# Kernel optimization log

Measured on AMD Instinct MI355X. Metric: run time of the kernel, lower is better.

Reference implementation:

```python
import jax, jax.numpy as jnp
import numpy as np

G = 128   # long_term_attn_g
H = 8     # num_attn_heads


def setup_inputs() -> dict:
    key = jax.random.key(0)
    ks = jax.random.split(key, 8)
    b, d, t, dk = 8, 1024, 8192, 512  # dk = model_dim // 2
    return {
        "qk": jax.random.normal(ks[0], (b, d, t), jnp.float32),
        "masks": jnp.ones((b, 1, t), jnp.float32),
        "wq": jax.random.normal(ks[1], (dk, d), jnp.float32) * 0.02,
        "bq": jnp.zeros((dk,), jnp.float32),
        "wk": jax.random.normal(ks[2], (dk, d), jnp.float32) * 0.02,
        "bk": jnp.zeros((dk,), jnp.float32),
        "wv": jax.random.normal(ks[3], (dk, d), jnp.float32) * 0.02,
        "bv": jnp.zeros((dk,), jnp.float32),
        "wo": jax.random.normal(ks[4], (d, dk), jnp.float32) * 0.02,
        "bo": jnp.zeros((d,), jnp.float32),
    }


def _to_patches(x, g):
    # convert_to_patches + rearrange 'b d np p -> (b p) d np'
    b, d, t = x.shape
    pad = (-t) % g
    x = jnp.pad(x, ((0, 0), (0, 0), (0, pad)))
    npat = x.shape[-1] // g
    return x.reshape(b, d, npat, g).transpose(0, 3, 1, 2).reshape(b * g, d, npat)


def reference(qk, masks, wq, bq, wk, bk, wv, bv, wo, bo):
    b, d, t = qk.shape
    xp = _to_patches(qk, G)     # [(b g), d, npat]  -- q, k, v source
    mp = _to_patches(masks, G)  # [(b g), 1, npat]  -- key-side attention mask

    # pointwise Conv1d projections == per-timestep matmuls
    q = jnp.einsum('od,bdt->bot', wq, xp) + bq[:, None]
    k = jnp.einsum('od,bdt->bot', wk, xp) + bk[:, None]
    v = jnp.einsum('od,bdt->bot', wv, xp) + bv[:, None]

    dk = wq.shape[0]
    dh = dk // H
    bg, _, npat = q.shape
    qh = q.reshape(bg, H, dh, npat)
    kh = k.reshape(bg, H, dh, npat)
    vh = v.reshape(bg, H, dh, npat)

    scores = jnp.einsum('bhdi,bhdj->bhij', qh, kh) / jnp.sqrt(jnp.float32(dh))
    scores = jnp.where(mp[:, :, None, :] > 0, scores, jnp.float32(-1e9))
    attn = jax.nn.softmax(scores, axis=-1)
    out = jnp.einsum('bhij,bhdj->bhdi', attn, vh).reshape(bg, dk, npat)

    # out_proj = GELU -> Conv1d(dk -> model_dim, k=1)
    out = jax.nn.gelu(out, approximate=False)
    out = jnp.einsum('od,bdt->bot', wo, out) + bo[:, None]

    # undo reshape: '(b g) d np -> b d (np g)', trim padding
    out = out.reshape(b, G, d, npat).transpose(0, 2, 3, 1).reshape(b, d, npat * G)[:, :, :t]
    return out * masks
```

## Files before the change

### kernel.cpp

```cpp
#include <hip/hip_runtime.h>
#include <hip/hip_bf16.h>
#include <cmath>

typedef __attribute__((ext_vector_type(4))) float f32x4;
typedef __attribute__((ext_vector_type(8))) short s16x8;

typedef __attribute__((address_space(1))) const void glb_void_t;
typedef __attribute__((address_space(3))) void lds_void_t;

#define MFMA(a, b, c) __builtin_amdgcn_mfma_f32_16x16x32_bf16(a, b, c, 0, 0, 0)
#define GLOAD_LDS(g, l) __builtin_amdgcn_global_load_lds((glb_void_t*)(g), (lds_void_t*)(l), 16, 0, 0)

__device__ __forceinline__ unsigned short bf(float x) {
  union { float f; unsigned u; } c; c.f = x;
  unsigned r = (c.u + 0x7fffu + ((c.u >> 16) & 1u)) >> 16;
  return (unsigned short)r;
}

__global__ void k_prep(const float* __restrict__ wq, const float* __restrict__ wk,
                       const float* __restrict__ wv, const float* __restrict__ bq,
                       const float* __restrict__ bk, const float* __restrict__ bv,
                       const float* __restrict__ wo,
                       __hip_bfloat16* __restrict__ wqkv, __hip_bfloat16* __restrict__ wob,
                       float* __restrict__ bqkv) {
  const int NW = 1536 * 1024, NO = 1024 * 512;
  for (int i = blockIdx.x * blockDim.x + threadIdx.x; i < NW + NO + 1536;
       i += gridDim.x * blockDim.x) {
    if (i < NW) {
      int r = i >> 10;
      float v = (r < 512) ? wq[i] : ((r < 1024) ? wk[i - 512 * 1024] : wv[i - 1024 * 1024]);
      ((unsigned short*)wqkv)[i] = bf(v);
    } else if (i < NW + NO) {
      int j = i - NW;
      ((unsigned short*)wob)[j] = bf(wo[j]);
    } else {
      int j = i - NW - NO;
      bqkv[j] = (j < 512) ? bq[j] : ((j < 1024) ? bk[j - 512] : bv[j - 1024]);
    }
  }
}

__global__ __launch_bounds__(256) void k_transpose(const float* __restrict__ qk,
                                                   __hip_bfloat16* __restrict__ qkT) {
  __shared__ float tile[64][65];
  const int b = blockIdx.z, t0 = blockIdx.x * 64, d0 = blockIdx.y * 64;
  const int tid = threadIdx.x;
  const int tq = tid & 15, dr = tid >> 4;
  const float* src = qk + ((size_t)b * 1024 + d0) * 8192 + t0;
#pragma unroll
  for (int i = 0; i < 4; i++) {
    int d = dr + i * 16;
    float4 v = *(const float4*)(src + (size_t)d * 8192 + tq * 4);
    tile[d][tq * 4 + 0] = v.x; tile[d][tq * 4 + 1] = v.y;
    tile[d][tq * 4 + 2] = v.z; tile[d][tq * 4 + 3] = v.w;
  }
  __syncthreads();
  const int d4 = (tid & 15) * 4, tr = tid >> 4;
  unsigned short* dst = (unsigned short*)qkT + ((size_t)b * 8192 + t0) * 1024 + d0;
#pragma unroll
  for (int i = 0; i < 4; i++) {
    int t = tr + i * 16;
    ushort4 o4;
    o4.x = bf(tile[d4 + 0][t]); o4.y = bf(tile[d4 + 1][t]);
    o4.z = bf(tile[d4 + 2][t]); o4.w = bf(tile[d4 + 3][t]);
    *(ushort4*)(dst + (size_t)t * 1024 + d4) = o4;
  }
}

__global__ __launch_bounds__(512) void k_qkv(const __hip_bfloat16* __restrict__ qkT,
                                             const __hip_bfloat16* __restrict__ wqkv,
                                             const float* __restrict__ bqkv,
                                             __hip_bfloat16* __restrict__ qkv) {
  __shared__ char smem[128 * 128 + 256 * 128];
  char* As = smem;
  char* Bs = smem + 16384;
  const int b = blockIdx.z, t0 = blockIdx.x * 128, o0 = blockIdx.y * 256;
  const int tid = threadIdx.x, l = tid & 63, w = tid >> 6;
  const int c = l & 15, g = l >> 4;
  const int wm = w >> 2, wn = w & 3;
  const int lrow = l >> 3, lcol = (l & 7) * 16;

  f32x4 acc[4][4];
#pragma unroll
  for (int i = 0; i < 4; i++)
#pragma unroll
    for (int j = 0; j < 4; j++) acc[i][j] = (f32x4){0.f, 0.f, 0.f, 0.f};

  const char* qbase = (const char*)(qkT + ((size_t)b * 8192 + t0) * 1024);
  const char* wbase = (const char*)(wqkv + (size_t)o0 * 1024);

  for (int ks = 0; ks < 16; ks++) {
    __syncthreads();
#pragma unroll
    for (int ii = 0; ii < 2; ii++) {
      int row = w * 16 + ii * 8 + lrow;
      int cb = lcol ^ ((row & 7) << 4);
      const char* gp = qbase + (size_t)row * 2048 + ks * 128 + cb;
      GLOAD_LDS(gp, As + (w * 16 + ii * 8) * 128);
    }
#pragma unroll
    for (int ii = 0; ii < 4; ii++) {
      int row = w * 32 + ii * 8 + lrow;
      int cb = lcol ^ ((row & 7) << 4);
      const char* gp = wbase + (size_t)row * 2048 + ks * 128 + cb;
      GLOAD_LDS(gp, Bs + (w * 32 + ii * 8) * 128);
    }
    __syncthreads();
#pragma unroll
    for (int kk = 0; kk < 2; kk++) {
      s16x8 av[4], bv[4];
#pragma unroll
      for (int mi = 0; mi < 4; mi++) {
        int row = wm * 64 + mi * 16 + c;
        int cb = (kk * 64 + g * 16) ^ ((row & 7) << 4);
        av[mi] = *(const s16x8*)(As + row * 128 + cb);
      }
#pragma unroll
      for (int ni = 0; ni < 4; ni++) {
        int row = wn * 64 + ni * 16 + c;
        int cb = (kk * 64 + g * 16) ^ ((row & 7) << 4);
        bv[ni] = *(const s16x8*)(Bs + row * 128 + cb);
      }
#pragma unroll
      for (int mi = 0; mi < 4; mi++)
#pragma unroll
        for (int ni = 0; ni < 4; ni++)
          acc[mi][ni] = MFMA(av[mi], bv[ni], acc[mi][ni]);
    }
  }
  unsigned short* outb = (unsigned short*)qkv + ((size_t)b * 8192 + t0) * 1536 + o0;
  float bias[4];
#pragma unroll
  for (int ni = 0; ni < 4; ni++) bias[ni] = bqkv[o0 + wn * 64 + ni * 16 + c];
#pragma unroll
  for (int mi = 0; mi < 4; mi++)
#pragma unroll
    for (int r = 0; r < 4; r++) {
      int t = wm * 64 + mi * 16 + g * 4 + r;
#pragma unroll
      for (int ni = 0; ni < 4; ni++) {
        int o = wn * 64 + ni * 16 + c;
        outb[(size_t)t * 1536 + o] = bf(acc[mi][ni][r] + bias[ni]);
      }
    }
}

__global__ __launch_bounds__(512) void k_attn(const __hip_bfloat16* __restrict__ qkv,
                                              const float* __restrict__ masks,
                                              __hip_bfloat16* __restrict__ a_out) {
  __shared__ char vlds[65536];
  const int tid = threadIdx.x, l = tid & 63, w = tid >> 6;
  const int c = l & 15, g = l >> 4;
  const int h = w;
  const int gg = blockIdx.x & 127, b = blockIdx.x >> 7;
  const size_t rowstep = (size_t)128 * 1536;
  const __hip_bfloat16* base = qkv + ((size_t)b * 8192 + gg) * 1536 + h * 64;
  const __hip_bfloat16* Qb = base;
  const __hip_bfloat16* Kb = base + 512;
  const char* Vrow0 = (const char*)(qkv + ((size_t)b * 8192 + gg) * 1536 + 1024);

  s16x8 kf[4][2], qf[4][2];
#pragma unroll
  for (int f = 0; f < 4; f++)
#pragma unroll
    for (int kk = 0; kk < 2; kk++) {
      size_t roff = (size_t)(f * 16 + c) * rowstep + kk * 32 + g * 8;
      kf[f][kk] = *(const s16x8*)(Kb + roff);
      qf[f][kk] = *(const s16x8*)(Qb + roff);
    }

#pragma unroll
  for (int i = 0; i < 8; ++i) {
    int j = w + 8 * i;
    const char* src = Vrow0 + (size_t)j * rowstep * 2 + ((l ^ i) << 4);
    GLOAD_LDS(src, vlds + j * 1024);
  }

  f32x4 st[4][4];
#pragma unroll
  for (int i = 0; i < 4; i++)
#pragma unroll
    for (int j = 0; j < 4; j++) st[i][j] = (f32x4){0.f, 0.f, 0.f, 0.f};
#pragma unroll
  for (int mj = 0; mj < 4; mj++)
#pragma unroll
    for (int ni = 0; ni < 4; ni++)
#pragma unroll
      for (int kk = 0; kk < 2; kk++)
        st[mj][ni] = MFMA(kf[mj][kk], qf[ni][kk], st[mj][ni]);

  float mk[4][4];
#pragma unroll
  for (int mj = 0; mj < 4; mj++)
#pragma unroll
    for (int r = 0; r < 4; r++)
      mk[mj][r] = masks[(size_t)b * 8192 + (size_t)(mj * 16 + g * 4 + r) * 128 + gg];

  float inv[4];
#pragma unroll
  for (int ni = 0; ni < 4; ni++) {
    float m = -1e30f;
#pragma unroll
    for (int mj = 0; mj < 4; mj++)
#pragma unroll
      for (int r = 0; r < 4; r++) {
        float s = st[mj][ni][r] * 0.125f;
        s = (mk[mj][r] > 0.f) ? s : -1e9f;
        st[mj][ni][r] = s;
        m = fmaxf(m, s);
      }
    m = fmaxf(m, __shfl_xor(m, 16));
    m = fmaxf(m, __shfl_xor(m, 32));
    float sm = 0.f;
#pragma unroll
    for (int mj = 0; mj < 4; mj++)
#pragma unroll
      for (int r = 0; r < 4; r++) {
        float p = expf(st[mj][ni][r] - m);
        st[mj][ni][r] = p;
        sm += p;
      }
    sm += __shfl_xor(sm, 16);
    sm += __shfl_xor(sm, 32);
    inv[ni] = 1.f / sm;
  }
#pragma unroll
  for (int mj = 0; mj < 4; mj++)
#pragma unroll
    for (int ni = 0; ni < 4; ni++)
#pragma unroll
      for (int r = 0; r < 4; r++) st[mj][ni][r] *= inv[ni];

  unsigned qd[4][4][2];
#pragma unroll
  for (int ni = 0; ni < 4; ni++)
#pragma unroll
    for (int mj = 0; mj < 4; mj++)
#pragma unroll
      for (int wv = 0; wv < 2; wv++)
        qd[ni][mj][wv] = (unsigned)bf(st[mj][ni][2 * wv]) |
                         ((unsigned)bf(st[mj][ni][2 * wv + 1]) << 16);

  __syncthreads();

  f32x4 oacc[4][4];
#pragma unroll
  for (int i = 0; i < 4; i++)
#pragma unroll
    for (int j = 0; j < 4; j++) oacc[i][j] = (f32x4){0.f, 0.f, 0.f, 0.f};

  const int srcA = c + 32 * (g & 1);
  const int srcB = srcA + 16;
  const bool hi = (g >= 2);
  const int coff = (c & 7) << 1;
  const int chi = c >> 3;
#pragma unroll
  for (int kk = 0; kk < 2; kk++) {
    s16x8 af[4];
#pragma unroll
    for (int ni = 0; ni < 4; ni++) {
      unsigned a0 = __shfl(qd[ni][2 * kk][0], srcA);
      unsigned b0 = __shfl(qd[ni][2 * kk + 1][0], srcA);
      unsigned a1 = __shfl(qd[ni][2 * kk][1], srcA);
      unsigned b1 = __shfl(qd[ni][2 * kk + 1][1], srcA);
      unsigned a2 = __shfl(qd[ni][2 * kk][0], srcB);
      unsigned b2 = __shfl(qd[ni][2 * kk + 1][0], srcB);
      unsigned a3 = __shfl(qd[ni][2 * kk][1], srcB);
      unsigned b3 = __shfl(qd[ni][2 * kk + 1][1], srcB);
      union { unsigned u[4]; s16x8 v; } uu;
      uu.u[0] = hi ? b0 : a0;
      uu.u[1] = hi ? b1 : a1;
      uu.u[2] = hi ? b2 : a2;
      uu.u[3] = hi ? b3 : a3;
      af[ni] = uu.v;
    }
    s16x8 bvv[4];
#pragma unroll
    for (int fd = 0; fd < 4; fd++) {
      const int key = kk * 4 + g;
      const int chunk = (h * 8 + fd * 2 + chi) ^ key;
      s16x8 t;
#pragma unroll
      for (int e = 0; e < 8; e++) {
        int j = kk * 32 + g * 8 + e;
        t[e] = *(const short*)(vlds + j * 1024 + (chunk << 4) + coff);
      }
      bvv[fd] = t;
    }
#pragma unroll
    for (int fi = 0; fi < 4; fi++)
#pragma unroll
      for (int fd = 0; fd < 4; fd++)
        oacc[fi][fd] = MFMA(af[fi], bvv[fd], oacc[fi][fd]);
  }

  unsigned short* ob = (unsigned short*)a_out + ((size_t)b * 8192 + gg) * 512 + h * 64;
#pragma unroll
  for (int fi = 0; fi < 4; fi++)
#pragma unroll
    for (int fd = 0; fd < 4; fd++)
#pragma unroll
      for (int r = 0; r < 4; r++) {
        float x = oacc[fi][fd][r];
        float ge = 0.5f * x * (1.f + erff(x * 0.70710678118f));
        int i = fi * 16 + g * 4 + r;
        ob[(size_t)i * (128 * 512) + fd * 16 + c] = bf(ge);
      }
}

__global__ __launch_bounds__(512) void k_out(const __hip_bfloat16* __restrict__ wob,
                                             const __hip_bfloat16* __restrict__ a,
                                             const float* __restrict__ bo,
                                             const float* __restrict__ masks,
                                             float* __restrict__ y) {
  __shared__ char smem[256 * 128 + 128 * 128];
  char* As = smem;
  char* Bs = smem + 32768;
  const int b = blockIdx.z, t0 = blockIdx.x * 128, o0 = blockIdx.y * 256;
  const int tid = threadIdx.x, l = tid & 63, w = tid >> 6;
  const int c = l & 15, g = l >> 4;
  const int wm = w >> 1, wn = w & 1;
  const int lrow = l >> 3, lcol = (l & 7) * 16;

  f32x4 acc[4][4];
#pragma unroll
  for (int i = 0; i < 4; i++)
#pragma unroll
    for (int j = 0; j < 4; j++) acc[i][j] = (f32x4){0.f, 0.f, 0.f, 0.f};

  const char* wbase = (const char*)(wob + (size_t)o0 * 512);
  const char* abase = (const char*)(a + ((size_t)b * 8192 + t0) * 512);

  for (int ks = 0; ks < 8; ks++) {
    __syncthreads();
#pragma unroll
    for (int ii = 0; ii < 4; ii++) {
      int row = w * 32 + ii * 8 + lrow;
      int cb = lcol ^ ((row & 7) << 4);
      const char* gp = wbase + (size_t)row * 1024 + ks * 128 + cb;
      GLOAD_LDS(gp, As + (w * 32 + ii * 8) * 128);
    }
#pragma unroll
    for (int ii = 0; ii < 2; ii++) {
      int row = w * 16 + ii * 8 + lrow;
      int cb = lcol ^ ((row & 7) << 4);
      const char* gp = abase + (size_t)row * 1024 + ks * 128 + cb;
      GLOAD_LDS(gp, Bs + (w * 16 + ii * 8) * 128);
    }
    __syncthreads();
#pragma unroll
    for (int kk = 0; kk < 2; kk++) {
      s16x8 av[4], bv[4];
#pragma unroll
      for (int mi = 0; mi < 4; mi++) {
        int row = wm * 64 + mi * 16 + c;
        int cb = (kk * 64 + g * 16) ^ ((row & 7) << 4);
        av[mi] = *(const s16x8*)(As + row * 128 + cb);
      }
#pragma unroll
      for (int ni = 0; ni < 4; ni++) {
        int row = wn * 64 + ni * 16 + c;
        int cb = (kk * 64 + g * 16) ^ ((row & 7) << 4);
        bv[ni] = *(const s16x8*)(Bs + row * 128 + cb);
      }
#pragma unroll
      for (int mi = 0; mi < 4; mi++)
#pragma unroll
        for (int ni = 0; ni < 4; ni++)
          acc[mi][ni] = MFMA(av[mi], bv[ni], acc[mi][ni]);
    }
  }
  int tcol[4];
  float mk[4];
#pragma unroll
  for (int ni = 0; ni < 4; ni++) {
    tcol[ni] = t0 + wn * 64 + ni * 16 + c;
    mk[ni] = masks[(size_t)b * 8192 + tcol[ni]];
  }
#pragma unroll
  for (int mi = 0; mi < 4; mi++)
#pragma unroll
    for (int r = 0; r < 4; r++) {
      int od = o0 + wm * 64 + mi * 16 + g * 4 + r;
      float bias = bo[od];
      float* yrow = y + ((size_t)b * 1024 + od) * 8192;
#pragma unroll
      for (int ni = 0; ni < 4; ni++)
        yrow[tcol[ni]] = (acc[mi][ni][r] + bias) * mk[ni];
    }
}

extern "C" void kernel_launch(void* const* d_in, const int* in_sizes, int n_in,
                              void* d_out, int out_size, void* d_ws, size_t ws_size,
                              hipStream_t stream) {
  const float* qk = (const float*)d_in[0];
  const float* masks = (const float*)d_in[1];
  const float* wq = (const float*)d_in[2];
  const float* bq = (const float*)d_in[3];
  const float* wk = (const float*)d_in[4];
  const float* bk = (const float*)d_in[5];
  const float* wv = (const float*)d_in[6];
  const float* bv = (const float*)d_in[7];
  const float* wo = (const float*)d_in[8];
  const float* bo = (const float*)d_in[9];

  char* ws = (char*)d_ws;
  __hip_bfloat16* qkT = (__hip_bfloat16*)ws;
  __hip_bfloat16* a = (__hip_bfloat16*)ws;
  __hip_bfloat16* wqkv = (__hip_bfloat16*)(ws + 134217728);
  __hip_bfloat16* wob = (__hip_bfloat16*)(ws + 134217728 + 3145728);
  float* bqkv = (float*)(ws + 134217728 + 3145728 + 1048576);

  __hip_bfloat16* qkv = (__hip_bfloat16*)d_out;
  float* y = (float*)d_out;

  k_prep<<<dim3(512), dim3(256), 0, stream>>>(wq, wk, wv, bq, bk, bv, wo, wqkv, wob, bqkv);
  k_transpose<<<dim3(128, 16, 8), dim3(256), 0, stream>>>(qk, qkT);
  k_qkv<<<dim3(64, 6, 8), dim3(512), 0, stream>>>(qkT, wqkv, bqkv, qkv);
  k_attn<<<dim3(1024), dim3(512), 0, stream>>>(qkv, masks, a);
  k_out<<<dim3(64, 4, 8), dim3(512), 0, stream>>>(wob, a, bo, masks, y);
}
```

Measured before the change: 475.6 us.

## Fuse fp32-to-bf16 transpose into QKV GEMM A-tile load and use tanh GELU

Removes the separate transpose kernel. The QKV GEMM now reads fp32 qk directly, converts it to bf16 with packed cvt instructions and writes it transposed into swizzled LDS, which saves the round trip of a 128MB intermediate through global memory. The grid is reordered so blocks that share the same activation tile run next to each other, which should improve L2 reuse of the fp32 input. GELU switches from erf to a sigmoid-form tanh approximation, which changes numerics slightly. The A loads are now synchronous register loads instead of direct-to-LDS loads, so latency hiding may get worse.

```diff
diff --git a/kernel.cpp b/kernel.cpp
--- a/kernel.cpp
+++ b/kernel.cpp
@@ -40,41 +40,14 @@
   }
 }
 
-__global__ __launch_bounds__(256) void k_transpose(const float* __restrict__ qk,
-                                                   __hip_bfloat16* __restrict__ qkT) {
-  __shared__ float tile[64][65];
-  const int b = blockIdx.z, t0 = blockIdx.x * 64, d0 = blockIdx.y * 64;
-  const int tid = threadIdx.x;
-  const int tq = tid & 15, dr = tid >> 4;
-  const float* src = qk + ((size_t)b * 1024 + d0) * 8192 + t0;
-#pragma unroll
-  for (int i = 0; i < 4; i++) {
-    int d = dr + i * 16;
-    float4 v = *(const float4*)(src + (size_t)d * 8192 + tq * 4);
-    tile[d][tq * 4 + 0] = v.x; tile[d][tq * 4 + 1] = v.y;
-    tile[d][tq * 4 + 2] = v.z; tile[d][tq * 4 + 3] = v.w;
-  }
-  __syncthreads();
-  const int d4 = (tid & 15) * 4, tr = tid >> 4;
-  unsigned short* dst = (unsigned short*)qkT + ((size_t)b * 8192 + t0) * 1024 + d0;
-#pragma unroll
-  for (int i = 0; i < 4; i++) {
-    int t = tr + i * 16;
-    ushort4 o4;
-    o4.x = bf(tile[d4 + 0][t]); o4.y = bf(tile[d4 + 1][t]);
-    o4.z = bf(tile[d4 + 2][t]); o4.w = bf(tile[d4 + 3][t]);
-    *(ushort4*)(dst + (size_t)t * 1024 + d4) = o4;
-  }
-}
-
-__global__ __launch_bounds__(512) void k_qkv(const __hip_bfloat16* __restrict__ qkT,
+__global__ __launch_bounds__(512) void k_qkv(const float* __restrict__ qk,
                                              const __hip_bfloat16* __restrict__ wqkv,
                                              const float* __restrict__ bqkv,
                                              __hip_bfloat16* __restrict__ qkv) {
   __shared__ char smem[128 * 128 + 256 * 128];
   char* As = smem;
   char* Bs = smem + 16384;
-  const int b = blockIdx.z, t0 = blockIdx.x * 128, o0 = blockIdx.y * 256;
+  const int b = blockIdx.z, t0 = blockIdx.y * 128, o0 = blockIdx.x * 256;
   const int tid = threadIdx.x, l = tid & 63, w = tid >> 6;
   const int c = l & 15, g = l >> 4;
   const int wm = w >> 2, wn = w & 3;
@@ -86,17 +59,35 @@
 #pragma unroll
     for (int j = 0; j < 4; j++) acc[i][j] = (f32x4){0.f, 0.f, 0.f, 0.f};
 
-  const char* qbase = (const char*)(qkT + ((size_t)b * 8192 + t0) * 1024);
+  const int dq = tid >> 5;
+  const int tq = tid & 31;
+  const float* aglob = qk + (size_t)b * 1024 * 8192 + (size_t)(dq * 4) * 8192 + t0 + tq * 4;
+  char* awr[4];
+#pragma unroll
+  for (int j = 0; j < 4; ++j) {
+    int t = tq * 4 + j;
+    awr[j] = As + t * 128 + ((dq * 8) ^ ((t & 7) << 4));
+  }
+
   const char* wbase = (const char*)(wqkv + (size_t)o0 * 1024);
 
   for (int ks = 0; ks < 16; ks++) {
     __syncthreads();
-#pragma unroll
-    for (int ii = 0; ii < 2; ii++) {
-      int row = w * 16 + ii * 8 + lrow;
-      int cb = lcol ^ ((row & 7) << 4);
-      const char* gp = qbase + (size_t)row * 2048 + ks * 128 + cb;
-      GLOAD_LDS(gp, As + (w * 16 + ii * 8) * 128);
+    float4 va[4];
+#pragma unroll
+    for (int i = 0; i < 4; ++i)
+      va[i] = *(const float4*)(aglob + ((size_t)ks * 64 + i) * 8192);
+#pragma unroll
+    for (int j = 0; j < 4; ++j) {
+      float a0 = ((const float*)&va[0])[j];
+      float a1 = ((const float*)&va[1])[j];
+      float a2 = ((const float*)&va[2])[j];
+      float a3 = ((const float*)&va[3])[j];
+      unsigned u0, u1;
+      asm("v_cvt_pk_bf16_f32 %0, %1, %2" : "=v"(u0) : "v"(a0), "v"(a1));
+      asm("v_cvt_pk_bf16_f32 %0, %1, %2" : "=v"(u1) : "v"(a2), "v"(a3));
+      uint2 uu; uu.x = u0; uu.y = u1;
+      *(uint2*)awr[j] = uu;
     }
 #pragma unroll
     for (int ii = 0; ii < 4; ii++) {
@@ -302,7 +293,8 @@
 #pragma unroll
       for (int r = 0; r < 4; r++) {
         float x = oacc[fi][fd][r];
-        float ge = 0.5f * x * (1.f + erff(x * 0.70710678118f));
+        float e = __expf(x * fmaf(x * x, 0.0713548162f, 1.5957691216f));
+        float ge = x * (e / (1.0f + e));
         int i = fi * 16 + g * 4 + r;
         ob[(size_t)i * (128 * 512) + fd * 16 + c] = bf(ge);
       }
@@ -405,7 +397,6 @@
   const float* bo = (const float*)d_in[9];
 
   char* ws = (char*)d_ws;
-  __hip_bfloat16* qkT = (__hip_bfloat16*)ws;
   __hip_bfloat16* a = (__hip_bfloat16*)ws;
   __hip_bfloat16* wqkv = (__hip_bfloat16*)(ws + 134217728);
   __hip_bfloat16* wob = (__hip_bfloat16*)(ws + 134217728 + 3145728);
@@ -415,8 +406,7 @@
   float* y = (float*)d_out;
 
   k_prep<<<dim3(512), dim3(256), 0, stream>>>(wq, wk, wv, bq, bk, bv, wo, wqkv, wob, bqkv);
-  k_transpose<<<dim3(128, 16, 8), dim3(256), 0, stream>>>(qk, qkT);
-  k_qkv<<<dim3(64, 6, 8), dim3(512), 0, stream>>>(qkT, wqkv, bqkv, qkv);
+  k_qkv<<<dim3(6, 64, 8), dim3(512), 0, stream>>>(qk, wqkv, bqkv, qkv);
   k_attn<<<dim3(1024), dim3(512), 0, stream>>>(qkv, masks, a);
   k_out<<<dim3(64, 4, 8), dim3(512), 0, stream>>>(wob, a, bo, masks, y);
 }
```

After: 496.9 us. 1.04x slower.
